# Optimization experiments

Hardware: AMD Instinct MI355X
Metric: run time of the kernel (lower is better)

Reference implementation:

```python
import jax, jax.numpy as jnp
import numpy as np

D_MODEL = 1024
D_INNER = 4096   # expand=4
D_STATE = 16
D_CONV = 4
DT_RANK = 64     # ceil(d_model/16)
BATCH = 2
SEQLEN = 2048


def setup_inputs() -> dict:
    key = jax.random.key(0)
    ks = jax.random.split(key, 9)
    s = 0.02
    x = jax.random.normal(ks[0], (BATCH, SEQLEN, D_MODEL), jnp.float32)
    in_proj_w = jax.random.normal(ks[1], (D_MODEL, 2 * D_INNER), jnp.float32) * s
    conv_w = jax.random.normal(ks[2], (D_INNER, D_CONV), jnp.float32) * 0.3
    conv_b = jax.random.normal(ks[3], (D_INNER,), jnp.float32) * 0.02
    x_proj_w = jax.random.normal(ks[4], (D_INNER, DT_RANK + 2 * D_STATE), jnp.float32) * s
    dt_proj_w = jax.random.normal(ks[5], (DT_RANK, D_INNER), jnp.float32) * (DT_RANK ** -0.5)
    dt_proj_b = jax.random.normal(ks[6], (D_INNER,), jnp.float32) * 0.1 - 4.0  # small softplus(dt)
    # A = repeat(arange(1, d_state+1)) as in mamba-ssm; A_log = log(A)
    A_log = jnp.log(jnp.broadcast_to(jnp.arange(1, D_STATE + 1, dtype=jnp.float32), (D_INNER, D_STATE)))
    D = jnp.ones((D_INNER,), jnp.float32)
    out_proj_w = jax.random.normal(ks[7], (D_INNER, D_MODEL), jnp.float32) * s
    return {"x": x, "in_proj_w": in_proj_w, "conv_w": conv_w, "conv_b": conv_b,
            "x_proj_w": x_proj_w, "dt_proj_w": dt_proj_w, "dt_proj_b": dt_proj_b,
            "A_log": A_log, "D": D, "out_proj_w": out_proj_w}


def reference(x, in_proj_w, conv_w, conv_b, x_proj_w, dt_proj_w, dt_proj_b, A_log, D, out_proj_w):
    Bsz, L, _ = x.shape
    # input projection -> (x branch, gate z), each [B, L, d_inner]
    xz = x @ in_proj_w
    xc, z = jnp.split(xz, 2, axis=-1)
    # causal depthwise conv1d, kernel D_CONV, left-padded
    xp = jnp.pad(xc, ((0, 0), (D_CONV - 1, 0), (0, 0)))
    xconv = conv_b + sum(xp[:, k:k + L, :] * conv_w[:, k] for k in range(D_CONV))
    xs = jax.nn.silu(xconv)  # [B, L, d_inner]
    # input-dependent SSM params
    proj = xs @ x_proj_w  # [B, L, dt_rank + 2*d_state]
    dt_lo, Bt, Ct = jnp.split(proj, [DT_RANK, DT_RANK + D_STATE], axis=-1)
    dt = jax.nn.softplus(dt_lo @ dt_proj_w + dt_proj_b)  # [B, L, d_inner]
    A = -jnp.exp(A_log)  # [d_inner, d_state]

    def step(h, inp):
        dt_t, B_t, C_t, u_t = inp  # [B,dI], [B,dS], [B,dS], [B,dI]
        dA = jnp.exp(dt_t[..., None] * A)                       # [B, dI, dS]
        h = h * dA + (dt_t * u_t)[..., None] * B_t[:, None, :]  # [B, dI, dS]
        y = jnp.einsum('bdn,bn->bd', h, C_t)                    # [B, dI]
        return h, y

    h0 = jnp.zeros((Bsz, D_INNER, D_STATE), x.dtype)
    inps = (dt.transpose(1, 0, 2), Bt.transpose(1, 0, 2),
            Ct.transpose(1, 0, 2), xs.transpose(1, 0, 2))
    _, ys = jax.lax.scan(step, h0, inps)  # ys: [L, B, d_inner]
    y = ys.transpose(1, 0, 2) + xs * D
    y = y * jax.nn.silu(z)
    return y @ out_proj_w
```

## Files before the change

kernel.cpp:

```cpp
#include <hip/hip_runtime.h>
#include <hip/hip_bf16.h>

#define D_MODEL 1024
#define D_INNER 4096
#define D_STATE 16
#define D_CONV 4
#define DT_RANK 64
#define BATCH 2
#define SEQLEN 2048
#define MROWS (BATCH * SEQLEN)
#define NPROJ (DT_RANK + 2 * D_STATE)
#define PST 128
#define NC 32
#define TC (SEQLEN / NC)
#define KSPLIT 8
#define KSP6 4

typedef unsigned short u16;
typedef unsigned int u32;
typedef __attribute__((ext_vector_type(8))) short short8;
typedef __attribute__((ext_vector_type(4))) float floatx4;
typedef __attribute__((ext_vector_type(16))) float floatx16;

#define LOG2E 1.44269504089f

__device__ __forceinline__ float bf2f(u16 u) {
    union { u32 i; float f; } v; v.i = ((u32)u) << 16; return v.f;
}
__device__ __forceinline__ u16 f2bf(float f) {
    union { float f; u32 i; } v; v.f = f;
    u32 x = v.i;
    u32 r = x + 0x7fffu + ((x >> 16) & 1u);
    return (u16)(r >> 16);
}
__device__ __forceinline__ float softplus_fast(float x) {
    float l = __logf(1.f + __expf(-fabsf(x)));
    return x > 0.f ? x + l : l;
}
__device__ __forceinline__ float sigmoid_fast(float x) {
    return __builtin_amdgcn_rcpf(1.f + __expf(-x));
}
__device__ __forceinline__ float exp2_hw(float x) {
    float r;
    asm("v_exp_f32 %0, %1" : "=v"(r) : "v"(x));
    return r;
}
__device__ __forceinline__ void pow_tree16(float r, float* pw) {
    pw[0] = r;
    pw[1] = r * r;
    pw[2] = pw[1] * r;
    pw[3] = pw[1] * pw[1];
    pw[4] = pw[3] * r;
    pw[5] = pw[3] * pw[1];
    pw[6] = pw[3] * pw[2];
    pw[7] = pw[3] * pw[3];
#pragma unroll
    for (int k = 0; k < 8; k++) pw[8 + k] = pw[7] * pw[k];
}
__device__ __forceinline__ void async_cp16(const u16* g, u16* l) {
    __builtin_amdgcn_global_load_lds((const __attribute__((address_space(1))) void*)g,
                                     (__attribute__((address_space(3))) void*)l, 16, 0, 0);
}

__global__ __launch_bounds__(256) void detect_dtype(const u16* __restrict__ x, int* __restrict__ flag,
                                                    int* __restrict__ sflag) {
    __shared__ int cnt;
    if (threadIdx.x == 0) { cnt = 0; *sflag = 0; }
    __syncthreads();
    int local = 0;
    for (int k = 0; k < 16; k++) {
        int e = threadIdx.x * 8192 + k * 512;
        u16 v = x[2 * e];
        int ex = (v >> 7) & 0xFF;
        if (ex >= 0x68 && ex <= 0x8F) local++;
    }
    atomicAdd(&cnt, local);
    __syncthreads();
    if (threadIdx.x == 0) *flag = (cnt >= 2458) ? 1 : 0;
}

__global__ __launch_bounds__(256) void ingest16(const void* __restrict__ src, u16* __restrict__ dst,
                                                int n, const int* __restrict__ flag) {
    int i = blockIdx.x * 256 + threadIdx.x;
    if (i >= n) return;
    if (*flag) dst[i] = ((const u16*)src)[i];
    else       dst[i] = f2bf(((const float*)src)[i]);
}

__global__ __launch_bounds__(256) void prep_small(const void* __restrict__ cw, const void* __restrict__ cb,
                                                  const void* __restrict__ dtb, const void* __restrict__ Dv,
                                                  const void* __restrict__ Alog,
                                                  u16* __restrict__ cw16, u16* __restrict__ cb16,
                                                  u16* __restrict__ dtb16, u16* __restrict__ D16,
                                                  float* __restrict__ A, const int* __restrict__ flag,
                                                  int* __restrict__ sflag) {
    int i = blockIdx.x * 256 + threadIdx.x;
    int isb = *flag;
    if (i < D_INNER * D_CONV)
        cw16[i] = isb ? ((const u16*)cw)[i] : f2bf(((const float*)cw)[i]);
    if (i < D_INNER) {
        cb16[i]  = isb ? ((const u16*)cb)[i]  : f2bf(((const float*)cb)[i]);
        dtb16[i] = isb ? ((const u16*)dtb)[i] : f2bf(((const float*)dtb)[i]);
        D16[i]   = isb ? ((const u16*)Dv)[i]  : f2bf(((const float*)Dv)[i]);
    }
    if (i < D_INNER * D_STATE) {
        float v = isb ? bf2f(((const u16*)Alog)[i]) : ((const float*)Alog)[i];
        float a = -expf(v);
        A[i] = a;
        float tgt = (float)((i & 15) + 1);
        if (fabsf(a + tgt) > 4e-6f * tgt) atomicOr(sflag, 1);
    }
}

__global__ __launch_bounds__(256) void transpose_w(const void* __restrict__ W, u16* __restrict__ WT,
                                                   int K, int N, const int* __restrict__ flag) {
    __shared__ float t[32][33];
    int k0 = blockIdx.y * 32, n0 = blockIdx.x * 32;
    int tid = threadIdx.x;
    int r = tid >> 3, c4 = (tid & 7) * 4;
    int isb = *flag;
    size_t base = (size_t)(k0 + r) * N + n0 + c4;
    float4 v;
    if (isb) { ushort4 u4 = *(const ushort4*)((const u16*)W + base);
               v = make_float4(bf2f(u4.x), bf2f(u4.y), bf2f(u4.z), bf2f(u4.w)); }
    else     { v = *(const float4*)((const float*)W + base); }
    t[c4 + 0][r] = v.x; t[c4 + 1][r] = v.y; t[c4 + 2][r] = v.z; t[c4 + 3][r] = v.w;
    __syncthreads();
    u16* o = WT + (size_t)(n0 + r) * K + k0 + c4;
    o[0] = f2bf(t[r][c4 + 0]);
    o[1] = f2bf(t[r][c4 + 1]);
    o[2] = f2bf(t[r][c4 + 2]);
    o[3] = f2bf(t[r][c4 + 3]);
}

template<int KS, int MODE>
__global__ __launch_bounds__(512, 2) void gemm8p(const u16* __restrict__ A, const u16* __restrict__ Bt,
                                                 u16* __restrict__ o0, u16* __restrict__ o1,
                                                 float* __restrict__ Pp) {
    __shared__ __align__(16) u16 lds[65536];
    const int tid = threadIdx.x;
    const int lane = tid & 63;
    const int wave = tid >> 6;
    const int wr = wave >> 2, wc = wave & 3;
    const int l31 = lane & 31, lhi = lane >> 5, sw = lane & 7;

    int m0, n0, kbase, kz;
    if (MODE == 0) {
        int wgid = (blockIdx.x & 7) * 64 + (blockIdx.x >> 3);
        m0 = (wgid & 15) * 256;
        n0 = (wgid >> 4) * 256;
        kbase = 0; kz = 0;
    } else {
        m0 = blockIdx.y * 256;
        n0 = blockIdx.x * 256;
        kz = blockIdx.z;
        kbase = kz * 1024;
    }
    const int NT = 1024 / 64;

    const int srow = tid >> 3;
    const int kswz = (((tid & 7) ^ (srow & 7)) << 3);
    const u16* pA = A + (size_t)(m0 + srow) * KS + kbase + kswz;
    const u16* pB = Bt + (size_t)(n0 + srow) * KS + kbase + kswz;

    const int k0f = (((0 + lhi) ^ sw) << 3);
    const int k1f = (((2 + lhi) ^ sw) << 3);
    const int k2f = (((4 + lhi) ^ sw) << 3);
    const int k3f = (((6 + lhi) ^ sw) << 3);
    const int aoff = (wr * 64 + l31) * 64;
    const int boff = (wc * 32 + l31) * 64;

    floatx16 acc[4][2];
#pragma unroll
    for (int i = 0; i < 4; i++)
#pragma unroll
        for (int j = 0; j < 2; j++) acc[i][j] = (floatx16)0.f;
    short8 af[2][4];
    short8 bfr[2][4];

#define STAGE_A(nb, h, kt) do { \
    const u16* g_ = pA + (size_t)(h) * 128 * KS + (kt) * 64; \
    u16* l_ = &lds[((nb) * 2 + (h)) * 8192 + tid * 8]; \
    async_cp16(g_, l_); \
    async_cp16(g_ + (size_t)64 * KS, l_ + 4096); \
} while (0)
#define STAGE_B(nb, h, kt) do { \
    const u16* g_ = pB + (size_t)(h) * 128 * KS + (kt) * 64; \
    u16* l_ = &lds[32768 + ((nb) * 2 + (h)) * 8192 + tid * 8]; \
    async_cp16(g_, l_); \
    async_cp16(g_ + (size_t)64 * KS, l_ + 4096); \
} while (0)
#define LOADA(b, h) do { \
    const u16* p_ = &lds[((b) * 2 + (h)) * 8192 + aoff]; \
    af[0][0] = *(const short8*)(p_ + k0f); \
    af[0][1] = *(const short8*)(p_ + k1f); \
    af[0][2] = *(const short8*)(p_ + k2f); \
    af[0][3] = *(const short8*)(p_ + k3f); \
    af[1][0] = *(const short8*)(p_ + 2048 + k0f); \
    af[1][1] = *(const short8*)(p_ + 2048 + k1f); \
    af[1][2] = *(const short8*)(p_ + 2048 + k2f); \
    af[1][3] = *(const short8*)(p_ + 2048 + k3f); \
} while (0)
#define LOADB(b, h) do { \
    const u16* p_ = &lds[32768 + ((b) * 2 + (h)) * 8192 + boff]; \
    bfr[h][0] = *(const short8*)(p_ + k0f); \
    bfr[h][1] = *(const short8*)(p_ + k1f); \
    bfr[h][2] = *(const short8*)(p_ + k2f); \
    bfr[h][3] = *(const short8*)(p_ + k3f); \
} while (0)
#define MFMAQ(qa, qb) do { \
    __builtin_amdgcn_s_setprio(1); \
    _Pragma("unroll") \
    for (int ii = 0; ii < 2; ii++) { \
        floatx16 c_ = acc[(qa) * 2 + ii][qb]; \
        c_ = __builtin_amdgcn_mfma_f32_32x32x16_bf16(af[ii][0], bfr[qb][0], c_, 0, 0, 0); \
        c_ = __builtin_amdgcn_mfma_f32_32x32x16_bf16(af[ii][1], bfr[qb][1], c_, 0, 0, 0); \
        c_ = __builtin_amdgcn_mfma_f32_32x32x16_bf16(af[ii][2], bfr[qb][2], c_, 0, 0, 0); \
        c_ = __builtin_amdgcn_mfma_f32_32x32x16_bf16(af[ii][3], bfr[qb][3], c_, 0, 0, 0); \
        acc[(qa) * 2 + ii][qb] = c_; \
    } \
    __builtin_amdgcn_s_setprio(0); \
} while (0)
#define VMW(N) asm volatile("s_waitcnt vmcnt(" #N ")" ::: "memory")
#define BARX() do { __builtin_amdgcn_s_barrier(); asm volatile("" ::: "memory"); } while (0)
#define SANDWICH() do { \
    __builtin_amdgcn_sched_barrier(0); \
    __builtin_amdgcn_s_barrier(); \
    asm volatile("s_waitcnt lgkmcnt(0)" ::: "memory"); \
    __builtin_amdgcn_sched_barrier(0); \
} while (0)

    STAGE_A(0, 0, 0);
    STAGE_B(0, 0, 0);
    STAGE_B(0, 1, 0);
    STAGE_A(0, 1, 0);
    VMW(4); BARX();

    for (int t = 0; t < NT - 1; ++t) {
        const int b = t & 1, nb = b ^ 1;
        LOADA(b, 0);
        LOADB(b, 0);
        STAGE_A(nb, 0, t + 1);
        SANDWICH();
        MFMAQ(0, 0);
        VMW(4); BARX();
        LOADB(b, 1);
        STAGE_B(nb, 0, t + 1);
        SANDWICH();
        MFMAQ(0, 1);
        VMW(4); BARX();
        LOADA(b, 1);
        STAGE_B(nb, 1, t + 1);
        SANDWICH();
        MFMAQ(1, 1);
        STAGE_A(nb, 1, t + 1);
        MFMAQ(1, 0);
        VMW(4); BARX();
    }
    {
        const int b = (NT - 1) & 1;
        LOADA(b, 0);
        LOADB(b, 0);
        SANDWICH();
        MFMAQ(0, 0);
        VMW(2); BARX();
        LOADB(b, 1);
        SANDWICH();
        MFMAQ(0, 1);
        VMW(0); BARX();
        LOADA(b, 1);
        MFMAQ(1, 1);
        MFMAQ(1, 0);
    }

    if constexpr (MODE == 0) {
        (void)kz; (void)Pp;
        u16* d = (n0 < D_INNER) ? o0 : o1;
        const int nb0 = (n0 < D_INNER) ? n0 : n0 - D_INNER;
#pragma unroll
        for (int i = 0; i < 4; i++) {
            const int rbase = m0 + (i >> 1) * 128 + wr * 64 + (i & 1) * 32 + lhi * 4;
#pragma unroll
            for (int j = 0; j < 2; j++) {
                const int ncol = nb0 + j * 128 + wc * 32 + l31;
#pragma unroll
                for (int reg = 0; reg < 16; reg++) {
                    const int row = rbase + (reg & 3) + ((reg >> 2) << 3);
                    d[(size_t)row * D_INNER + ncol] = f2bf(acc[i][j][reg]);
                }
            }
        }
    } else {
        (void)o0; (void)o1;
        float* d = Pp + (size_t)kz * MROWS * D_MODEL;
#pragma unroll
        for (int i = 0; i < 4; i++) {
            const int rbase = m0 + (i >> 1) * 128 + wr * 64 + (i & 1) * 32 + lhi * 4;
#pragma unroll
            for (int j = 0; j < 2; j++) {
                const int ncol = n0 + j * 128 + wc * 32 + l31;
#pragma unroll
                for (int reg = 0; reg < 16; reg++) {
                    const int row = rbase + (reg & 3) + ((reg >> 2) << 3);
                    d[(size_t)row * D_MODEL + ncol] = acc[i][j][reg];
                }
            }
        }
    }
#undef STAGE_A
#undef STAGE_B
#undef LOADA
#undef LOADB
#undef MFMAQ
#undef VMW
#undef BARX
#undef SANDWICH
}

__global__ __launch_bounds__(256) void reduce_out(const float* __restrict__ Pp, void* __restrict__ out,
                                                  const int* __restrict__ flag) {
    int i = (blockIdx.x * 256 + threadIdx.x) * 4;
    float4 s = *(const float4*)&Pp[i];
#pragma unroll
    for (int z = 1; z < KSP6; z++) {
        float4 p = *(const float4*)&Pp[(size_t)z * MROWS * D_MODEL + i];
        s.x += p.x; s.y += p.y; s.z += p.z; s.w += p.w;
    }
    if (*flag) {
        ushort4 o = make_ushort4(f2bf(s.x), f2bf(s.y), f2bf(s.z), f2bf(s.w));
        *(ushort4*)((u16*)out + i) = o;
    } else {
        *(float4*)((float*)out + i) = s;
    }
}

__global__ __launch_bounds__(256) void gemm_proj(const u16* __restrict__ A, const u16* __restrict__ Bt,
                                                 float* __restrict__ Pp) {
    const int K = D_INNER;
    __shared__ __align__(16) u16 sA[128 * 32];
    __shared__ __align__(16) u16 sB[128 * 32];
    int tid = threadIdx.x;
    int lane = tid & 63;
    int wave = tid >> 6;
    int wm = (wave >> 1) * 64, wn = (wave & 1) * 64;
    int quad = lane >> 4, l15 = lane & 15;
    int m0 = blockIdx.y * 128;
    int kz = blockIdx.x;
    int kbase = kz * (K / KSPLIT);

    floatx4 acc[4][4];
#pragma unroll
    for (int i = 0; i < 4; i++)
#pragma unroll
        for (int j = 0; j < 4; j++) acc[i][j] = (floatx4)0.f;

    const u16* ga0 = A + (size_t)(m0 + (tid >> 2)) * K + (tid & 3) * 8;
    const u16* ga1 = A + (size_t)(m0 + 64 + (tid >> 2)) * K + (tid & 3) * 8;
    const u16* gb0 = Bt + (size_t)(tid >> 2) * K + (tid & 3) * 8;
    const u16* gb1 = Bt + (size_t)(64 + (tid >> 2)) * K + (tid & 3) * 8;
    u16* la0 = &sA[tid * 8];
    u16* la1 = &sA[(256 + tid) * 8];
    u16* lb0 = &sB[tid * 8];
    u16* lb1 = &sB[(256 + tid) * 8];

    for (int k0 = kbase; k0 < kbase + K / KSPLIT; k0 += 32) {
        async_cp16(ga0 + k0, la0);
        async_cp16(ga1 + k0, la1);
        async_cp16(gb0 + k0, lb0);
        async_cp16(gb1 + k0, lb1);
        __syncthreads();
        short8 af[4], bf[4];
#pragma unroll
        for (int i = 0; i < 4; i++) {
            af[i] = *(const short8*)&sA[(wm + i * 16 + l15) * 32 + quad * 8];
            bf[i] = *(const short8*)&sB[(wn + i * 16 + l15) * 32 + quad * 8];
        }
#pragma unroll
        for (int i = 0; i < 4; i++)
#pragma unroll
            for (int j = 0; j < 4; j++)
                acc[i][j] = __builtin_amdgcn_mfma_f32_16x16x32_bf16(af[i], bf[j], acc[i][j], 0, 0, 0);
        __syncthreads();
    }

    float* d = Pp + (size_t)kz * MROWS * PST;
#pragma unroll
    for (int i = 0; i < 4; i++)
#pragma unroll
        for (int j = 0; j < 4; j++)
#pragma unroll
            for (int r = 0; r < 4; r++) {
                int mm = m0 + wm + i * 16 + quad * 4 + r;
                int nn = wn + j * 16 + l15;
                d[(size_t)mm * PST + nn] = acc[i][j][r];
            }
}

__global__ __launch_bounds__(256) void reduce_proj(const float* __restrict__ Pp, float* __restrict__ proj,
                                                   u16* __restrict__ proj_lo) {
    int i = blockIdx.x * 256 + threadIdx.x;
    float s = 0.f;
#pragma unroll
    for (int z = 0; z < KSPLIT; z++) s += Pp[(size_t)z * MROWS * PST + i];
    proj[i] = s;
    int col = i & (PST - 1);
    if (col < DT_RANK) proj_lo[(size_t)(i >> 7) * DT_RANK + col] = f2bf(s);
}

__global__ __launch_bounds__(256) void gemm_dt(const u16* __restrict__ A, const u16* __restrict__ Bt,
                                               const u16* __restrict__ dtb, u16* __restrict__ dt) {
    const int K = DT_RANK;
    __shared__ __align__(16) u16 smem[64 * 132];
    u16* sA = smem;
    u16* sB = smem + 128 * 32;
    int tid = threadIdx.x;
    int lane = tid & 63;
    int wave = tid >> 6;
    int wm = (wave >> 1) * 64, wn = (wave & 1) * 64;
    int quad = lane >> 4, l15 = lane & 15;
    int m0 = blockIdx.y * 128, n0 = blockIdx.x * 128;

    floatx4 acc[4][4];
#pragma unroll
    for (int i = 0; i < 4; i++)
#pragma unroll
        for (int j = 0; j < 4; j++) acc[i][j] = (floatx4)0.f;

    const u16* ga0 = A + (size_t)(m0 + (tid >> 2)) * K + (tid & 3) * 8;
    const u16* ga1 = A + (size_t)(m0 + 64 + (tid >> 2)) * K + (tid & 3) * 8;
    const u16* gb0 = Bt + (size_t)(n0 + (tid >> 2)) * K + (tid & 3) * 8;
    const u16* gb1 = Bt + (size_t)(n0 + 64 + (tid >> 2)) * K + (tid & 3) * 8;
    u16* la0 = &sA[tid * 8];
    u16* la1 = &sA[(256 + tid) * 8];
    u16* lb0 = &sB[tid * 8];
    u16* lb1 = &sB[(256 + tid) * 8];

    for (int k0 = 0; k0 < K; k0 += 32) {
        async_cp16(ga0 + k0, la0);
        async_cp16(ga1 + k0, la1);
        async_cp16(gb0 + k0, lb0);
        async_cp16(gb1 + k0, lb1);
        __syncthreads();
        short8 af[4], bf[4];
#pragma unroll
        for (int i = 0; i < 4; i++) {
            af[i] = *(const short8*)&sA[(wm + i * 16 + l15) * 32 + quad * 8];
            bf[i] = *(const short8*)&sB[(wn + i * 16 + l15) * 32 + quad * 8];
        }
#pragma unroll
        for (int i = 0; i < 4; i++)
#pragma unroll
            for (int j = 0; j < 4; j++)
                acc[i][j] = __builtin_amdgcn_mfma_f32_16x16x32_bf16(af[i], bf[j], acc[i][j], 0, 0, 0);
        __syncthreads();
    }

#pragma unroll
    for (int h = 0; h < 2; h++) {
        __syncthreads();
        if (wm == h * 64) {
#pragma unroll
            for (int j = 0; j < 4; j++) {
                int col = wn + j * 16 + l15;
                float b = bf2f(dtb[n0 + col]);
#pragma unroll
                for (int i = 0; i < 4; i++)
#pragma unroll
                    for (int r = 0; r < 4; r++) {
                        int row = i * 16 + quad * 4 + r;
                        smem[row * 132 + col] = f2bf(softplus_fast(acc[i][j][r] + b));
                    }
            }
        }
        __syncthreads();
#pragma unroll
        for (int p = 0; p < 4; p++) {
            int row = p * 16 + (tid >> 4);
            int chunk = tid & 15;
            uint4 v = *(const uint4*)&smem[row * 132 + chunk * 8];
            *(uint4*)&dt[(size_t)(m0 + h * 64 + row) * D_INNER + n0 + chunk * 8] = v;
        }
    }
}

__global__ __launch_bounds__(256) void conv_silu(const u16* __restrict__ xc, const u16* __restrict__ cw,
                                                 const u16* __restrict__ cb, u16* __restrict__ xs) {
    int idx = blockIdx.x * 256 + threadIdx.x;
    int g = idx & (D_INNER / 8 - 1);
    int bt = idx >> 9;
    int t = bt & (SEQLEN - 1);
    int d0 = g * 8;
    size_t row = (size_t)bt * D_INNER + d0;
    u16 wv[32];
    *(uint4*)&wv[0]  = *(const uint4*)&cw[d0 * 4];
    *(uint4*)&wv[8]  = *(const uint4*)&cw[d0 * 4 + 8];
    *(uint4*)&wv[16] = *(const uint4*)&cw[d0 * 4 + 16];
    *(uint4*)&wv[24] = *(const uint4*)&cw[d0 * 4 + 24];
    u16 cbv[8];
    *(uint4*)&cbv[0] = *(const uint4*)&cb[d0];
    u16 x0[8] = {0, 0, 0, 0, 0, 0, 0, 0};
    u16 x1[8] = {0, 0, 0, 0, 0, 0, 0, 0};
    u16 x2[8] = {0, 0, 0, 0, 0, 0, 0, 0};
    u16 x3[8];
    if (t >= 3) *(uint4*)x0 = *(const uint4*)&xc[row - 3 * (size_t)D_INNER];
    if (t >= 2) *(uint4*)x1 = *(const uint4*)&xc[row - 2 * (size_t)D_INNER];
    if (t >= 1) *(uint4*)x2 = *(const uint4*)&xc[row - 1 * (size_t)D_INNER];
    *(uint4*)x3 = *(const uint4*)&xc[row];
    u16 out[8];
#pragma unroll
    for (int ch = 0; ch < 8; ch++) {
        float a = bf2f(cbv[ch]);
        a += bf2f(x0[ch]) * bf2f(wv[ch * 4 + 0]);
        a += bf2f(x1[ch]) * bf2f(wv[ch * 4 + 1]);
        a += bf2f(x2[ch]) * bf2f(wv[ch * 4 + 2]);
        a += bf2f(x3[ch]) * bf2f(wv[ch * 4 + 3]);
        out[ch] = f2bf(a * sigmoid_fast(a));
    }
    *(uint4*)&xs[row] = *(const uint4*)&out[0];
}

__global__ __launch_bounds__(256) void scan_phase1(const float* __restrict__ proj, const u16* __restrict__ dt,
                                                   const float* __restrict__ A, const u16* __restrict__ xs,
                                                   float* __restrict__ hloc, float* __restrict__ Ssum,
                                                   const int* __restrict__ sflag) {
    int d = blockIdx.x * 256 + threadIdx.x;
    int c = blockIdx.y, b = blockIdx.z;
    int t0 = c * TC;
    int structured = (*sflag == 0);
    float h[16];
#pragma unroll
    for (int n = 0; n < 16; n++) h[n] = 0.f;
    float S = 0.f;
    size_t base = ((size_t)b * SEQLEN + t0) * D_INNER + d;
    const float* prow = proj + ((size_t)b * SEQLEN + t0) * PST + DT_RANK;
    u16 dcur = dt[base], ucur = xs[base];
    if (structured) {
        for (int t = 0; t < TC; t++) {
            size_t nidx = base + (size_t)((t + 1 < TC) ? t + 1 : t) * D_INNER;
            u16 dnxt = dt[nidx];
            u16 unxt = xs[nidx];
            float4 B0 = *(const float4*)(prow + t * PST + 0);
            float4 B1 = *(const float4*)(prow + t * PST + 4);
            float4 B2 = *(const float4*)(prow + t * PST + 8);
            float4 B3 = *(const float4*)(prow + t * PST + 12);
            float dtv = bf2f(dcur), u = bf2f(ucur);
            S += dtv;
            float du = dtv * u;
            float Bf[16] = {B0.x, B0.y, B0.z, B0.w, B1.x, B1.y, B1.z, B1.w,
                            B2.x, B2.y, B2.z, B2.w, B3.x, B3.y, B3.z, B3.w};
            float pw[16];
            pow_tree16(exp2_hw(-LOG2E * dtv), pw);
#pragma unroll
            for (int n = 0; n < 16; n++)
                h[n] = h[n] * pw[n] + du * Bf[n];
            dcur = dnxt; ucur = unxt;
        }
    } else {
        float Areg[16];
        const float4* Ap = (const float4*)(A + (size_t)d * 16);
#pragma unroll
        for (int n = 0; n < 4; n++) {
            float4 v = Ap[n];
            Areg[n * 4 + 0] = v.x * LOG2E; Areg[n * 4 + 1] = v.y * LOG2E;
            Areg[n * 4 + 2] = v.z * LOG2E; Areg[n * 4 + 3] = v.w * LOG2E;
        }
        for (int t = 0; t < TC; t++) {
            size_t nidx = base + (size_t)((t + 1 < TC) ? t + 1 : t) * D_INNER;
            u16 dnxt = dt[nidx];
            u16 unxt = xs[nidx];
            float4 B0 = *(const float4*)(prow + t * PST + 0);
            float4 B1 = *(const float4*)(prow + t * PST + 4);
            float4 B2 = *(const float4*)(prow + t * PST + 8);
            float4 B3 = *(const float4*)(prow + t * PST + 12);
            float dtv = bf2f(dcur), u = bf2f(ucur);
            S += dtv;
            float du = dtv * u;
            float Bf[16] = {B0.x, B0.y, B0.z, B0.w, B1.x, B1.y, B1.z, B1.w,
                            B2.x, B2.y, B2.z, B2.w, B3.x, B3.y, B3.z, B3.w};
#pragma unroll
            for (int n = 0; n < 16; n++)
                h[n] = h[n] * exp2_hw(dtv * Areg[n]) + du * Bf[n];
            dcur = dnxt; ucur = unxt;
        }
    }
    float* hp = &hloc[(((size_t)b * NC + c) * D_INNER + d) * 16];
#pragma unroll
    for (int n = 0; n < 16; n += 4)
        *(float4*)&hp[n] = make_float4(h[n], h[n + 1], h[n + 2], h[n + 3]);
    Ssum[((size_t)b * NC + c) * D_INNER + d] = S;
}

__global__ __launch_bounds__(256) void scan_phase2(const float* __restrict__ A, const float* __restrict__ Ssum,
                                                   float* __restrict__ hloc) {
    int tid = blockIdx.x * 256 + threadIdx.x;
    int n = tid & 15;
    int d = (tid >> 4) & (D_INNER - 1);
    int b = tid >> 16;
    float An2 = A[d * 16 + n] * LOG2E;
    float h = 0.f;
    for (int c = 0; c < NC; c++) {
        size_t idx = (((size_t)b * NC + c) * D_INNER + d) * 16 + n;
        float hl = hloc[idx];
        float S = Ssum[((size_t)b * NC + c) * D_INNER + d];
        hloc[idx] = h;
        h = hl + h * exp2_hw(An2 * S);
    }
}

__global__ __launch_bounds__(256) void scan_phase3(const float* __restrict__ proj, const u16* __restrict__ dt,
                                                   const float* __restrict__ A, const u16* __restrict__ D16,
                                                   const float* __restrict__ hinit, const u16* __restrict__ z16,
                                                   u16* __restrict__ xs, const int* __restrict__ sflag) {
    int d = blockIdx.x * 256 + threadIdx.x;
    int c = blockIdx.y, b = blockIdx.z;
    int t0 = c * TC;
    int structured = (*sflag == 0);
    float h[16];
    {
        const float* hp = &hinit[(((size_t)b * NC + c) * D_INNER + d) * 16];
#pragma unroll
        for (int n = 0; n < 16; n += 4) {
            float4 v = *(const float4*)&hp[n];
            h[n] = v.x; h[n + 1] = v.y; h[n + 2] = v.z; h[n + 3] = v.w;
        }
    }
    float Dd = bf2f(D16[d]);
    size_t base = ((size_t)b * SEQLEN + t0) * D_INNER + d;
    const float* prow = proj + ((size_t)b * SEQLEN + t0) * PST + DT_RANK;
    u16 dcur = dt[base], ucur = xs[base], zcur = z16[base];
    if (structured) {
        for (int t = 0; t < TC; t++) {
            size_t nidx = base + (size_t)((t + 1 < TC) ? t + 1 : t) * D_INNER;
            u16 dnxt = dt[nidx];
            u16 unxt = xs[nidx];
            u16 znxt = z16[nidx];
            float4 B0 = *(const float4*)(prow + t * PST + 0);
            float4 B1 = *(const float4*)(prow + t * PST + 4);
            float4 B2 = *(const float4*)(prow + t * PST + 8);
            float4 B3 = *(const float4*)(prow + t * PST + 12);
            float4 C0 = *(const float4*)(prow + t * PST + 16);
            float4 C1 = *(const float4*)(prow + t * PST + 20);
            float4 C2 = *(const float4*)(prow + t * PST + 24);
            float4 C3 = *(const float4*)(prow + t * PST + 28);
            float dtv = bf2f(dcur), u = bf2f(ucur), zv = bf2f(zcur);
            float du = dtv * u;
            float Bf[16] = {B0.x, B0.y, B0.z, B0.w, B1.x, B1.y, B1.z, B1.w,
                            B2.x, B2.y, B2.z, B2.w, B3.x, B3.y, B3.z, B3.w};
            float Cf[16] = {C0.x, C0.y, C0.z, C0.w, C1.x, C1.y, C1.z, C1.w,
                            C2.x, C2.y, C2.z, C2.w, C3.x, C3.y, C3.z, C3.w};
            float pw[16];
            pow_tree16(exp2_hw(-LOG2E * dtv), pw);
            float y = 0.f;
#pragma unroll
            for (int n = 0; n < 16; n++) {
                h[n] = h[n] * pw[n] + du * Bf[n];
                y += h[n] * Cf[n];
            }
            float gate = zv * sigmoid_fast(zv);
            xs[base + (size_t)t * D_INNER] = f2bf((y + u * Dd) * gate);
            dcur = dnxt; ucur = unxt; zcur = znxt;
        }
    } else {
        float Areg[16];
        const float4* Ap = (const float4*)(A + (size_t)d * 16);
#pragma unroll
        for (int n = 0; n < 4; n++) {
            float4 v = Ap[n];
            Areg[n * 4 + 0] = v.x * LOG2E; Areg[n * 4 + 1] = v.y * LOG2E;
            Areg[n * 4 + 2] = v.z * LOG2E; Areg[n * 4 + 3] = v.w * LOG2E;
        }
        for (int t = 0; t < TC; t++) {
            size_t nidx = base + (size_t)((t + 1 < TC) ? t + 1 : t) * D_INNER;
            u16 dnxt = dt[nidx];
            u16 unxt = xs[nidx];
            u16 znxt = z16[nidx];
            float4 B0 = *(const float4*)(prow + t * PST + 0);
            float4 B1 = *(const float4*)(prow + t * PST + 4);
            float4 B2 = *(const float4*)(prow + t * PST + 8);
            float4 B3 = *(const float4*)(prow + t * PST + 12);
            float4 C0 = *(const float4*)(prow + t * PST + 16);
            float4 C1 = *(const float4*)(prow + t * PST + 20);
            float4 C2 = *(const float4*)(prow + t * PST + 24);
            float4 C3 = *(const float4*)(prow + t * PST + 28);
            float dtv = bf2f(dcur), u = bf2f(ucur), zv = bf2f(zcur);
            float du = dtv * u;
            float Bf[16] = {B0.x, B0.y, B0.z, B0.w, B1.x, B1.y, B1.z, B1.w,
                            B2.x, B2.y, B2.z, B2.w, B3.x, B3.y, B3.z, B3.w};
            float Cf[16] = {C0.x, C0.y, C0.z, C0.w, C1.x, C1.y, C1.z, C1.w,
                            C2.x, C2.y, C2.z, C2.w, C3.x, C3.y, C3.z, C3.w};
            float y = 0.f;
#pragma unroll
            for (int n = 0; n < 16; n++) {
                h[n] = h[n] * exp2_hw(dtv * Areg[n]) + du * Bf[n];
                y += h[n] * Cf[n];
            }
            float gate = zv * sigmoid_fast(zv);
            xs[base + (size_t)t * D_INNER] = f2bf((y + u * Dd) * gate);
            dcur = dnxt; ucur = unxt; zcur = znxt;
        }
    }
}

extern "C" void kernel_launch(void* const* d_in, const int* in_sizes, int n_in,
                              void* d_out, int out_size, void* d_ws, size_t ws_size,
                              hipStream_t stream) {
    const void* x          = d_in[0];
    const void* in_proj_w  = d_in[1];
    const void* conv_w     = d_in[2];
    const void* conv_b     = d_in[3];
    const void* x_proj_w   = d_in[4];
    const void* dt_proj_w  = d_in[5];
    const void* dt_proj_b  = d_in[6];
    const void* A_log      = d_in[7];
    const void* Dvec       = d_in[8];
    const void* out_proj_w = d_in[9];

    char* w = (char*)d_ws;
    const size_t MB = 1024 * 1024;
    const size_t KB = 1024;
    int*   flag    = (int*)(w + 0);
    int*   sflag   = (int*)(w + 16);
    float* Aws     = (float*)(w + 1 * KB);
    float* proj    = (float*)(w + 1 * MB);
    u16*   cw16    = (u16*)(w + 3 * MB);
    u16*   cb16    = (u16*)(w + 3 * MB + 64 * KB);
    u16*   dtb16   = (u16*)(w + 3 * MB + 128 * KB);
    u16*   D16     = (u16*)(w + 3 * MB + 192 * KB);
    u16*   proj_lo = (u16*)(w + 3 * MB + 512 * KB);
    u16*   dtwT    = (u16*)(w + 4 * MB);
    u16*   buf1    = (u16*)(w + 5 * MB);
    u16*   dt16    = buf1;
    u16*   zbuf    = (u16*)(w + 37 * MB);
    float* Pp6     = (float*)(w + 5 * MB);
    u16*   xs      = (u16*)(w + 69 * MB);
    u16*   x16     = (u16*)(w + 101 * MB);
    u16*   ipwT    = (u16*)(w + 110 * MB);
    float* Pp      = (float*)(w + 101 * MB);
    float* hloc    = (float*)(w + 101 * MB);
    float* Ssum    = (float*)(w + 117 * MB);
    u16*   opwT    = (u16*)(w + 127 * MB);
    u16*   xpwT    = (u16*)(w + 136 * MB);

    detect_dtype<<<dim3(1), dim3(256), 0, stream>>>((const u16*)x, flag, sflag);
    prep_small<<<dim3(256), dim3(256), 0, stream>>>(conv_w, conv_b, dt_proj_b, Dvec, A_log,
                                                    cw16, cb16, dtb16, D16, Aws, flag, sflag);
    ingest16<<<dim3(MROWS * D_MODEL / 256), dim3(256), 0, stream>>>(x, x16, MROWS * D_MODEL, flag);
    transpose_w<<<dim3(2 * D_INNER / 32, D_MODEL / 32), dim3(256), 0, stream>>>(in_proj_w, ipwT, D_MODEL, 2 * D_INNER, flag);
    transpose_w<<<dim3(D_MODEL / 32, D_INNER / 32), dim3(256), 0, stream>>>(out_proj_w, opwT, D_INNER, D_MODEL, flag);
    transpose_w<<<dim3(NPROJ / 32, D_INNER / 32), dim3(256), 0, stream>>>(x_proj_w, xpwT, D_INNER, NPROJ, flag);
    transpose_w<<<dim3(D_INNER / 32, DT_RANK / 32), dim3(256), 0, stream>>>(dt_proj_w, dtwT, DT_RANK, D_INNER, flag);

    gemm8p<1024, 0><<<dim3(512), dim3(512), 0, stream>>>(x16, ipwT, buf1, zbuf, nullptr);
    conv_silu<<<dim3(MROWS * D_INNER / 8 / 256), dim3(256), 0, stream>>>(buf1, cw16, cb16, xs);
    gemm_proj<<<dim3(KSPLIT, MROWS / 128), dim3(256), 0, stream>>>(xs, xpwT, Pp);
    reduce_proj<<<dim3(MROWS * PST / 256), dim3(256), 0, stream>>>(Pp, proj, proj_lo);
    gemm_dt<<<dim3(D_INNER / 128, MROWS / 128), dim3(256), 0, stream>>>(proj_lo, dtwT, dtb16, dt16);
    scan_phase1<<<dim3(D_INNER / 256, NC, BATCH), dim3(256), 0, stream>>>(proj, dt16, Aws, xs, hloc, Ssum, sflag);
    scan_phase2<<<dim3(BATCH * D_INNER * D_STATE / 256), dim3(256), 0, stream>>>(Aws, Ssum, hloc);
    scan_phase3<<<dim3(D_INNER / 256, NC, BATCH), dim3(256), 0, stream>>>(proj, dt16, Aws, D16, hloc, zbuf, xs, sflag);
    gemm8p<4096, 1><<<dim3(D_MODEL / 256, MROWS / 256, KSP6), dim3(512), 0, stream>>>(xs, opwT, nullptr, nullptr, Pp6);
    reduce_out<<<dim3(MROWS * D_MODEL / 1024), dim3(256), 0, stream>>>(Pp6, d_out, flag);
}
```

Before: 430.4 us.

## Load GEMM B operand directly from global into registers, switch to 16x16x32 MFMA

```diff
diff --git a/kernel.cpp b/kernel.cpp
--- a/kernel.cpp
+++ b/kernel.cpp
@@ -20,7 +20,6 @@
 typedef unsigned int u32;
 typedef __attribute__((ext_vector_type(8))) short short8;
 typedef __attribute__((ext_vector_type(4))) float floatx4;
-typedef __attribute__((ext_vector_type(16))) float floatx16;
 
 #define LOG2E 1.44269504089f
 
@@ -137,12 +136,12 @@
 __global__ __launch_bounds__(512, 2) void gemm8p(const u16* __restrict__ A, const u16* __restrict__ Bt,
                                                  u16* __restrict__ o0, u16* __restrict__ o1,
                                                  float* __restrict__ Pp) {
-    __shared__ __align__(16) u16 lds[65536];
+    __shared__ __align__(16) u16 lds[32768];
     const int tid = threadIdx.x;
     const int lane = tid & 63;
     const int wave = tid >> 6;
     const int wr = wave >> 2, wc = wave & 3;
-    const int l31 = lane & 31, lhi = lane >> 5, sw = lane & 7;
+    const int quad = lane >> 4, l15 = lane & 15;
 
     int m0, n0, kbase, kz;
     if (MODE == 0) {
@@ -161,22 +160,21 @@
     const int srow = tid >> 3;
     const int kswz = (((tid & 7) ^ (srow & 7)) << 3);
     const u16* pA = A + (size_t)(m0 + srow) * KS + kbase + kswz;
-    const u16* pB = Bt + (size_t)(n0 + srow) * KS + kbase + kswz;
-
-    const int k0f = (((0 + lhi) ^ sw) << 3);
-    const int k1f = (((2 + lhi) ^ sw) << 3);
-    const int k2f = (((4 + lhi) ^ sw) << 3);
-    const int k3f = (((6 + lhi) ^ sw) << 3);
-    const int aoff = (wr * 64 + l31) * 64;
-    const int boff = (wc * 32 + l31) * 64;
-
-    floatx16 acc[4][2];
-#pragma unroll
-    for (int i = 0; i < 4; i++)
-#pragma unroll
-        for (int j = 0; j < 2; j++) acc[i][j] = (floatx16)0.f;
-    short8 af[2][4];
-    short8 bfr[2][4];
+
+    const int rsw = (l15 & 7) << 3;
+    const int ksel0 = (quad * 8) ^ rsw;
+    const int ksel1 = (32 + quad * 8) ^ rsw;
+    const int aoff = (wr * 64 + l15) * 64;
+
+    const u16* gB = Bt + (size_t)(n0 + wc * 64 + l15) * KS + kbase + quad * 8;
+
+    floatx4 acc[8][4];
+#pragma unroll
+    for (int i = 0; i < 8; i++)
+#pragma unroll
+        for (int j = 0; j < 4; j++) acc[i][j] = (floatx4)0.f;
+    short8 af[4][2];
+    short8 bfr[4][2];
 
 #define STAGE_A(nb, h, kt) do { \
     const u16* g_ = pA + (size_t)(h) * 128 * KS + (kt) * 64; \
@@ -184,93 +182,60 @@
     async_cp16(g_, l_); \
     async_cp16(g_ + (size_t)64 * KS, l_ + 4096); \
 } while (0)
-#define STAGE_B(nb, h, kt) do { \
-    const u16* g_ = pB + (size_t)(h) * 128 * KS + (kt) * 64; \
-    u16* l_ = &lds[32768 + ((nb) * 2 + (h)) * 8192 + tid * 8]; \
-    async_cp16(g_, l_); \
-    async_cp16(g_ + (size_t)64 * KS, l_ + 4096); \
-} while (0)
 #define LOADA(b, h) do { \
     const u16* p_ = &lds[((b) * 2 + (h)) * 8192 + aoff]; \
-    af[0][0] = *(const short8*)(p_ + k0f); \
-    af[0][1] = *(const short8*)(p_ + k1f); \
-    af[0][2] = *(const short8*)(p_ + k2f); \
-    af[0][3] = *(const short8*)(p_ + k3f); \
-    af[1][0] = *(const short8*)(p_ + 2048 + k0f); \
-    af[1][1] = *(const short8*)(p_ + 2048 + k1f); \
-    af[1][2] = *(const short8*)(p_ + 2048 + k2f); \
-    af[1][3] = *(const short8*)(p_ + 2048 + k3f); \
+    _Pragma("unroll") \
+    for (int ii = 0; ii < 4; ii++) { \
+        af[ii][0] = *(const short8*)(p_ + ii * 1024 + ksel0); \
+        af[ii][1] = *(const short8*)(p_ + ii * 1024 + ksel1); \
+    } \
 } while (0)
-#define LOADB(b, h) do { \
-    const u16* p_ = &lds[32768 + ((b) * 2 + (h)) * 8192 + boff]; \
-    bfr[h][0] = *(const short8*)(p_ + k0f); \
-    bfr[h][1] = *(const short8*)(p_ + k1f); \
-    bfr[h][2] = *(const short8*)(p_ + k2f); \
-    bfr[h][3] = *(const short8*)(p_ + k3f); \
+#define BLOAD(kt) do { \
+    _Pragma("unroll") \
+    for (int j = 0; j < 4; j++) { \
+        const u16* q_ = gB + (size_t)j * 16 * KS + (size_t)(kt) * 64; \
+        bfr[j][0] = *(const short8*)(q_); \
+        bfr[j][1] = *(const short8*)(q_ + 32); \
+    } \
 } while (0)
-#define MFMAQ(qa, qb) do { \
+#define MFMAP(ph) do { \
     __builtin_amdgcn_s_setprio(1); \
     _Pragma("unroll") \
-    for (int ii = 0; ii < 2; ii++) { \
-        floatx16 c_ = acc[(qa) * 2 + ii][qb]; \
-        c_ = __builtin_amdgcn_mfma_f32_32x32x16_bf16(af[ii][0], bfr[qb][0], c_, 0, 0, 0); \
-        c_ = __builtin_amdgcn_mfma_f32_32x32x16_bf16(af[ii][1], bfr[qb][1], c_, 0, 0, 0); \
-        c_ = __builtin_amdgcn_mfma_f32_32x32x16_bf16(af[ii][2], bfr[qb][2], c_, 0, 0, 0); \
-        c_ = __builtin_amdgcn_mfma_f32_32x32x16_bf16(af[ii][3], bfr[qb][3], c_, 0, 0, 0); \
-        acc[(qa) * 2 + ii][qb] = c_; \
+    for (int ii = 0; ii < 4; ii++) \
+    _Pragma("unroll") \
+    for (int j = 0; j < 4; j++) { \
+        floatx4 c_ = acc[(ph) * 4 + ii][j]; \
+        c_ = __builtin_amdgcn_mfma_f32_16x16x32_bf16(af[ii][0], bfr[j][0], c_, 0, 0, 0); \
+        c_ = __builtin_amdgcn_mfma_f32_16x16x32_bf16(af[ii][1], bfr[j][1], c_, 0, 0, 0); \
+        acc[(ph) * 4 + ii][j] = c_; \
     } \
     __builtin_amdgcn_s_setprio(0); \
 } while (0)
 #define VMW(N) asm volatile("s_waitcnt vmcnt(" #N ")" ::: "memory")
 #define BARX() do { __builtin_amdgcn_s_barrier(); asm volatile("" ::: "memory"); } while (0)
-#define SANDWICH() do { \
-    __builtin_amdgcn_sched_barrier(0); \
-    __builtin_amdgcn_s_barrier(); \
-    asm volatile("s_waitcnt lgkmcnt(0)" ::: "memory"); \
-    __builtin_amdgcn_sched_barrier(0); \
-} while (0)
-
+
+    BLOAD(0);
     STAGE_A(0, 0, 0);
-    STAGE_B(0, 0, 0);
-    STAGE_B(0, 1, 0);
     STAGE_A(0, 1, 0);
-    VMW(4); BARX();
+    VMW(0); BARX();
 
     for (int t = 0; t < NT - 1; ++t) {
         const int b = t & 1, nb = b ^ 1;
         LOADA(b, 0);
-        LOADB(b, 0);
         STAGE_A(nb, 0, t + 1);
-        SANDWICH();
-        MFMAQ(0, 0);
-        VMW(4); BARX();
-        LOADB(b, 1);
-        STAGE_B(nb, 0, t + 1);
-        SANDWICH();
-        MFMAQ(0, 1);
-        VMW(4); BARX();
+        MFMAP(0);
         LOADA(b, 1);
-        STAGE_B(nb, 1, t + 1);
-        SANDWICH();
-        MFMAQ(1, 1);
         STAGE_A(nb, 1, t + 1);
-        MFMAQ(1, 0);
-        VMW(4); BARX();
+        MFMAP(1);
+        BLOAD(t + 1);
+        VMW(8); BARX();
     }
     {
         const int b = (NT - 1) & 1;
         LOADA(b, 0);
-        LOADB(b, 0);
-        SANDWICH();
-        MFMAQ(0, 0);
-        VMW(2); BARX();
-        LOADB(b, 1);
-        SANDWICH();
-        MFMAQ(0, 1);
-        VMW(0); BARX();
+        MFMAP(0);
         LOADA(b, 1);
-        MFMAQ(1, 1);
-        MFMAQ(1, 0);
+        MFMAP(1);
     }
 
     if constexpr (MODE == 0) {
@@ -278,43 +243,37 @@
         u16* d = (n0 < D_INNER) ? o0 : o1;
         const int nb0 = (n0 < D_INNER) ? n0 : n0 - D_INNER;
 #pragma unroll
-        for (int i = 0; i < 4; i++) {
-            const int rbase = m0 + (i >> 1) * 128 + wr * 64 + (i & 1) * 32 + lhi * 4;
-#pragma unroll
-            for (int j = 0; j < 2; j++) {
-                const int ncol = nb0 + j * 128 + wc * 32 + l31;
-#pragma unroll
-                for (int reg = 0; reg < 16; reg++) {
-                    const int row = rbase + (reg & 3) + ((reg >> 2) << 3);
-                    d[(size_t)row * D_INNER + ncol] = f2bf(acc[i][j][reg]);
-                }
+        for (int i = 0; i < 8; i++) {
+            const int mrow = m0 + (i >> 2) * 128 + wr * 64 + (i & 3) * 16 + quad * 4;
+#pragma unroll
+            for (int j = 0; j < 4; j++) {
+                const int ncol = nb0 + wc * 64 + j * 16 + l15;
+#pragma unroll
+                for (int r = 0; r < 4; r++)
+                    d[(size_t)(mrow + r) * D_INNER + ncol] = f2bf(acc[i][j][r]);
             }
         }
     } else {
         (void)o0; (void)o1;
         float* d = Pp + (size_t)kz * MROWS * D_MODEL;
 #pragma unroll
-        for (int i = 0; i < 4; i++) {
-            const int rbase = m0 + (i >> 1) * 128 + wr * 64 + (i & 1) * 32 + lhi * 4;
-#pragma unroll
-            for (int j = 0; j < 2; j++) {
-                const int ncol = n0 + j * 128 + wc * 32 + l31;
-#pragma unroll
-                for (int reg = 0; reg < 16; reg++) {
-                    const int row = rbase + (reg & 3) + ((reg >> 2) << 3);
-                    d[(size_t)row * D_MODEL + ncol] = acc[i][j][reg];
-                }
+        for (int i = 0; i < 8; i++) {
+            const int mrow = m0 + (i >> 2) * 128 + wr * 64 + (i & 3) * 16 + quad * 4;
+#pragma unroll
+            for (int j = 0; j < 4; j++) {
+                const int ncol = n0 + wc * 64 + j * 16 + l15;
+#pragma unroll
+                for (int r = 0; r < 4; r++)
+                    d[(size_t)(mrow + r) * D_MODEL + ncol] = acc[i][j][r];
             }
         }
     }
 #undef STAGE_A
-#undef STAGE_B
 #undef LOADA
-#undef LOADB
-#undef MFMAQ
+#undef BLOAD
+#undef MFMAP
 #undef VMW
 #undef BARX
-#undef SANDWICH
 }
 
 __global__ __launch_bounds__(256) void reduce_out(const float* __restrict__ Pp, void* __restrict__ out,
```

New measurement: 476.0 us. 10.6% more time.

## Switch GEMM to 16x16x32 MFMA and stage bf16 epilogue through LDS

Applied to the files above, without the earlier changes.

```diff
diff --git a/kernel.cpp b/kernel.cpp
--- a/kernel.cpp
+++ b/kernel.cpp
@@ -20,7 +20,6 @@
 typedef unsigned int u32;
 typedef __attribute__((ext_vector_type(8))) short short8;
 typedef __attribute__((ext_vector_type(4))) float floatx4;
-typedef __attribute__((ext_vector_type(16))) float floatx16;
 
 #define LOG2E 1.44269504089f
 
@@ -142,7 +141,7 @@
     const int lane = tid & 63;
     const int wave = tid >> 6;
     const int wr = wave >> 2, wc = wave & 3;
-    const int l31 = lane & 31, lhi = lane >> 5, sw = lane & 7;
+    const int quad = lane >> 4, l15 = lane & 15;
 
     int m0, n0, kbase, kz;
     if (MODE == 0) {
@@ -163,20 +162,19 @@
     const u16* pA = A + (size_t)(m0 + srow) * KS + kbase + kswz;
     const u16* pB = Bt + (size_t)(n0 + srow) * KS + kbase + kswz;
 
-    const int k0f = (((0 + lhi) ^ sw) << 3);
-    const int k1f = (((2 + lhi) ^ sw) << 3);
-    const int k2f = (((4 + lhi) ^ sw) << 3);
-    const int k3f = (((6 + lhi) ^ sw) << 3);
-    const int aoff = (wr * 64 + l31) * 64;
-    const int boff = (wc * 32 + l31) * 64;
-
-    floatx16 acc[4][2];
-#pragma unroll
-    for (int i = 0; i < 4; i++)
-#pragma unroll
-        for (int j = 0; j < 2; j++) acc[i][j] = (floatx16)0.f;
-    short8 af[2][4];
-    short8 bfr[2][4];
+    const int rsw = (l15 & 7) << 3;
+    const int ksel0 = (quad * 8) ^ rsw;
+    const int ksel1 = (32 + quad * 8) ^ rsw;
+    const int aoff = (wr * 64 + l15) * 64;
+    const int boff = (wc * 32 + l15) * 64;
+
+    floatx4 acc[8][4];
+#pragma unroll
+    for (int i = 0; i < 8; i++)
+#pragma unroll
+        for (int j = 0; j < 4; j++) acc[i][j] = (floatx4)0.f;
+    short8 af[4][2];
+    short8 bfr[2][2][2];
 
 #define STAGE_A(nb, h, kt) do { \
     const u16* g_ = pA + (size_t)(h) * 128 * KS + (kt) * 64; \
@@ -192,32 +190,30 @@
 } while (0)
 #define LOADA(b, h) do { \
     const u16* p_ = &lds[((b) * 2 + (h)) * 8192 + aoff]; \
-    af[0][0] = *(const short8*)(p_ + k0f); \
-    af[0][1] = *(const short8*)(p_ + k1f); \
-    af[0][2] = *(const short8*)(p_ + k2f); \
-    af[0][3] = *(const short8*)(p_ + k3f); \
-    af[1][0] = *(const short8*)(p_ + 2048 + k0f); \
-    af[1][1] = *(const short8*)(p_ + 2048 + k1f); \
-    af[1][2] = *(const short8*)(p_ + 2048 + k2f); \
-    af[1][3] = *(const short8*)(p_ + 2048 + k3f); \
+    _Pragma("unroll") \
+    for (int ii = 0; ii < 4; ii++) { \
+        af[ii][0] = *(const short8*)(p_ + ii * 1024 + ksel0); \
+        af[ii][1] = *(const short8*)(p_ + ii * 1024 + ksel1); \
+    } \
 } while (0)
 #define LOADB(b, h) do { \
     const u16* p_ = &lds[32768 + ((b) * 2 + (h)) * 8192 + boff]; \
-    bfr[h][0] = *(const short8*)(p_ + k0f); \
-    bfr[h][1] = *(const short8*)(p_ + k1f); \
-    bfr[h][2] = *(const short8*)(p_ + k2f); \
-    bfr[h][3] = *(const short8*)(p_ + k3f); \
+    _Pragma("unroll") \
+    for (int jj = 0; jj < 2; jj++) { \
+        bfr[h][jj][0] = *(const short8*)(p_ + jj * 1024 + ksel0); \
+        bfr[h][jj][1] = *(const short8*)(p_ + jj * 1024 + ksel1); \
+    } \
 } while (0)
 #define MFMAQ(qa, qb) do { \
     __builtin_amdgcn_s_setprio(1); \
     _Pragma("unroll") \
-    for (int ii = 0; ii < 2; ii++) { \
-        floatx16 c_ = acc[(qa) * 2 + ii][qb]; \
-        c_ = __builtin_amdgcn_mfma_f32_32x32x16_bf16(af[ii][0], bfr[qb][0], c_, 0, 0, 0); \
-        c_ = __builtin_amdgcn_mfma_f32_32x32x16_bf16(af[ii][1], bfr[qb][1], c_, 0, 0, 0); \
-        c_ = __builtin_amdgcn_mfma_f32_32x32x16_bf16(af[ii][2], bfr[qb][2], c_, 0, 0, 0); \
-        c_ = __builtin_amdgcn_mfma_f32_32x32x16_bf16(af[ii][3], bfr[qb][3], c_, 0, 0, 0); \
-        acc[(qa) * 2 + ii][qb] = c_; \
+    for (int ii = 0; ii < 4; ii++) \
+    _Pragma("unroll") \
+    for (int jj = 0; jj < 2; jj++) { \
+        floatx4 c_ = acc[(qa) * 4 + ii][(qb) * 2 + jj]; \
+        c_ = __builtin_amdgcn_mfma_f32_16x16x32_bf16(af[ii][0], bfr[qb][jj][0], c_, 0, 0, 0); \
+        c_ = __builtin_amdgcn_mfma_f32_16x16x32_bf16(af[ii][1], bfr[qb][jj][1], c_, 0, 0, 0); \
+        acc[(qa) * 4 + ii][(qb) * 2 + jj] = c_; \
     } \
     __builtin_amdgcn_s_setprio(0); \
 } while (0)
@@ -277,33 +273,50 @@
         (void)kz; (void)Pp;
         u16* d = (n0 < D_INNER) ? o0 : o1;
         const int nb0 = (n0 < D_INNER) ? n0 : n0 - D_INNER;
-#pragma unroll
-        for (int i = 0; i < 4; i++) {
-            const int rbase = m0 + (i >> 1) * 128 + wr * 64 + (i & 1) * 32 + lhi * 4;
-#pragma unroll
-            for (int j = 0; j < 2; j++) {
-                const int ncol = nb0 + j * 128 + wc * 32 + l31;
-#pragma unroll
-                for (int reg = 0; reg < 16; reg++) {
-                    const int row = rbase + (reg & 3) + ((reg >> 2) << 3);
-                    d[(size_t)row * D_INNER + ncol] = f2bf(acc[i][j][reg]);
+        asm volatile("s_waitcnt lgkmcnt(0)" ::: "memory");
+        BARX();
+        u16* wbase = &lds[wave * 4608];
+#pragma unroll
+        for (int p = 0; p < 2; p++) {
+#pragma unroll
+            for (int i = 0; i < 4; i++) {
+                const int lro = i * 16 + quad * 4;
+#pragma unroll
+                for (int j = 0; j < 4; j++) {
+                    const int lc = (j >> 1) * 32 + (j & 1) * 16 + l15;
+#pragma unroll
+                    for (int r = 0; r < 4; r++)
+                        wbase[(lro + r) * 72 + lc] = f2bf(acc[p * 4 + i][j][r]);
                 }
             }
+            asm volatile("s_waitcnt lgkmcnt(0)" ::: "memory");
+            __builtin_amdgcn_sched_barrier(0);
+            const int gr = m0 + p * 128 + wr * 64 + lane;
+#pragma unroll
+            for (int c = 0; c < 2; c++) {
+                const u16* src = &wbase[lane * 72 + c * 32];
+                u16* dst = &d[(size_t)gr * D_INNER + nb0 + c * 128 + wc * 32];
+#pragma unroll
+                for (int q = 0; q < 4; q++) {
+                    short8 v = *(const short8*)(src + q * 8);
+                    *(short8*)(dst + q * 8) = v;
+                }
+            }
+            asm volatile("s_waitcnt lgkmcnt(0)" ::: "memory");
+            __builtin_amdgcn_sched_barrier(0);
         }
     } else {
         (void)o0; (void)o1;
         float* d = Pp + (size_t)kz * MROWS * D_MODEL;
 #pragma unroll
-        for (int i = 0; i < 4; i++) {
-            const int rbase = m0 + (i >> 1) * 128 + wr * 64 + (i & 1) * 32 + lhi * 4;
-#pragma unroll
-            for (int j = 0; j < 2; j++) {
-                const int ncol = n0 + j * 128 + wc * 32 + l31;
-#pragma unroll
-                for (int reg = 0; reg < 16; reg++) {
-                    const int row = rbase + (reg & 3) + ((reg >> 2) << 3);
-                    d[(size_t)row * D_MODEL + ncol] = acc[i][j][reg];
-                }
+        for (int i = 0; i < 8; i++) {
+            const int mrow = m0 + wr * 64 + (i & 3) * 16 + (i >> 2) * 128 + quad * 4;
+#pragma unroll
+            for (int j = 0; j < 4; j++) {
+                const int ncol = n0 + wc * 32 + (j & 1) * 16 + (j >> 1) * 128 + l15;
+#pragma unroll
+                for (int r = 0; r < 4; r++)
+                    d[(size_t)(mrow + r) * D_MODEL + ncol] = acc[i][j][r];
             }
         }
     }
```

Result: no change. 438.3 us (+1.8%).
